# Kernel optimization log

Hardware: AMD Instinct MI355X
Metric: run time of the kernel (lower is better)

## Reference

```python
import jax, jax.numpy as jnp
import numpy as np

N, E, B = 16000, 256000, 32
IN, HID, H1, OUT, H2 = 768, 256, 4, 128, 2
LN_EPS = 1e-5


def _gat_layer(x, src, dst, W, a_src, a_dst, b, heads, out, n, concat):
    # x: (n, in), W: (heads*out, in), a_src/a_dst: (heads, out), b: (heads*out,) or (out,)
    h = (x @ W.T).reshape(n, heads, out)                      # (n, H, out)
    alpha_s = (h * a_src).sum(-1)                             # (n, H)
    alpha_d = (h * a_dst).sum(-1)                             # (n, H)
    e = jax.nn.leaky_relu(alpha_s[src] + alpha_d[dst], 0.2)   # (E', H)
    # segment softmax over incoming edges of each dst node
    m = jax.ops.segment_max(e, dst, num_segments=n)           # (n, H)
    ex = jnp.exp(e - m[dst])
    den = jax.ops.segment_sum(ex, dst, num_segments=n)
    alpha = ex / (den[dst] + 1e-16)                           # (E', H)
    msg = h[src] * alpha[..., None]                           # (E', H, out)
    agg = jax.ops.segment_sum(msg, dst, num_segments=n)       # (n, H, out)
    o = agg.reshape(n, heads * out) if concat else agg.mean(axis=1)
    return o + b


def setup_inputs() -> dict:
    key = jax.random.key(0)
    ks = jax.random.split(key, 16)
    x = jax.random.normal(ks[0], (N, IN), dtype=jnp.float32)
    edge_index = jax.random.randint(ks[1], (2, E), 0, N, dtype=jnp.int32)
    batch = jnp.sort(jax.random.randint(ks[2], (N,), 0, B, dtype=jnp.int32))
    s = 0.05
    return {
        "x": x, "edge_index": edge_index, "batch": batch,
        "W1": jax.random.normal(ks[3], (H1 * HID, IN), jnp.float32) * s,
        "a1_src": jax.random.normal(ks[4], (H1, HID), jnp.float32) * s,
        "a1_dst": jax.random.normal(ks[5], (H1, HID), jnp.float32) * s,
        "b1": jnp.zeros((H1 * HID,), jnp.float32),
        "W2": jax.random.normal(ks[6], (H2 * OUT, H1 * HID), jnp.float32) * s,
        "a2_src": jax.random.normal(ks[7], (H2, OUT), jnp.float32) * s,
        "a2_dst": jax.random.normal(ks[8], (H2, OUT), jnp.float32) * s,
        "b2": jnp.zeros((OUT,), jnp.float32),
        "proj_W": jax.random.normal(ks[9], (768, OUT), jnp.float32) * s,
        "proj_b": jnp.zeros((768,), jnp.float32),
        "ln_g": jnp.ones((768,), jnp.float32),
        "ln_b": jnp.zeros((768,), jnp.float32),
    }


def reference(x, edge_index, batch, W1, a1_src, a1_dst, b1,
              W2, a2_src, a2_dst, b2, proj_W, proj_b, ln_g, ln_b):
    # add self-loops (PyG GATConv default add_self_loops=True)
    loop = jnp.arange(N, dtype=edge_index.dtype)
    src = jnp.concatenate([edge_index[0], loop])
    dst = jnp.concatenate([edge_index[1], loop])

    h1 = jax.nn.elu(_gat_layer(x, src, dst, W1, a1_src, a1_dst, b1, H1, HID, N, True))
    # dropout = 0 (eval mode)
    h2 = jax.nn.elu(_gat_layer(h1, src, dst, W2, a2_src, a2_dst, b2, H2, OUT, N, False))

    # global mean pool per graph
    sums = jax.ops.segment_sum(h2, batch, num_segments=B)            # (B, OUT)
    cnt = jax.ops.segment_sum(jnp.ones((N,), h2.dtype), batch, num_segments=B)
    pooled = sums / jnp.maximum(cnt, 1.0)[:, None]

    z = pooled @ proj_W.T + proj_b                                   # (B, 768)
    mu = z.mean(-1, keepdims=True)
    var = ((z - mu) ** 2).mean(-1, keepdims=True)
    graph_embed = (z - mu) / jnp.sqrt(var + LN_EPS) * ln_g + ln_b
    return graph_embed, h2
```

## Files before the change

### kernel.cpp

```cpp
#include <hip/hip_runtime.h>
#include <cstddef>

#define NN   16000
#define NE   256000
#define EP   (NE + NN)
#define BG   32
#define IN_F 768
#define HID  256
#define H1C  4
#define F1   (H1C * HID)
#define OUTF 128
#define H2C  2
#define F2   (H2C * OUTF)

typedef __bf16 bf16x8 __attribute__((ext_vector_type(8)));
typedef float  f32x4  __attribute__((ext_vector_type(4)));
typedef float  f32x2  __attribute__((ext_vector_type(2)));
typedef unsigned short us8 __attribute__((ext_vector_type(8)));

static __device__ __forceinline__ float lrelu02(float x) { return x > 0.f ? x : 0.2f * x; }
static __device__ __forceinline__ float eluf(float x)    { return x > 0.f ? x : expm1f(x); }
static __device__ __forceinline__ unsigned short rne_bf16(float f) {
    unsigned u = __float_as_uint(f);
    return (unsigned short)((u + 0x7fffu + ((u >> 16) & 1u)) >> 16);
}
static __device__ __forceinline__ float b2f(unsigned short u) {
    return __uint_as_float(((unsigned)u) << 16);
}
static __device__ __forceinline__ f32x2 cvt2(unsigned int u) {
    f32x2 r;
    r.x = __uint_as_float(u << 16);
    r.y = __uint_as_float(u & 0xffff0000u);
    return r;
}

#define GLDS16(gp, lp) __builtin_amdgcn_global_load_lds(                         \
    (const __attribute__((address_space(1))) void*)(gp),                          \
    (__attribute__((address_space(3))) void*)(lp), 16, 0, 0)

#define NB_X  ((NN * IN_F) / 1024)
#define NB_W1 ((F1 * IN_F) / 1024)
#define NB_W2 ((F2 * F1) / 1024)
#define NB_H  ((EP + 255) / 256)
#define NB_PREP (NB_X + NB_W1 + NB_W2 + NB_H)

static __device__ __forceinline__ void f2b_body(const float* __restrict__ in,
                                                unsigned short* __restrict__ out,
                                                int blk, int t) {
    int i = (blk * 256 + t) * 4;
    float4 v = *(const float4*)&in[i];
    ushort4 o;
    o.x = rne_bf16(v.x); o.y = rne_bf16(v.y); o.z = rne_bf16(v.z); o.w = rne_bf16(v.w);
    *(ushort4*)&out[i] = o;
}

__global__ __launch_bounds__(256) void k_prep(const float* __restrict__ x,
                                              const float* __restrict__ W1,
                                              const float* __restrict__ W2,
                                              unsigned short* __restrict__ xb,
                                              unsigned short* __restrict__ W1b,
                                              unsigned short* __restrict__ W2b,
                                              const int* __restrict__ ei,
                                              int* __restrict__ deg) {
    int b = blockIdx.x, t = threadIdx.x;
    if (b < NB_X) { f2b_body(x, xb, b, t); return; }
    b -= NB_X;
    if (b < NB_W1) { f2b_body(W1, W1b, b, t); return; }
    b -= NB_W1;
    if (b < NB_W2) { f2b_body(W2, W2b, b, t); return; }
    b -= NB_W2;
    int e = b * 256 + t;
    if (e >= EP) return;
    int d = (e < NE) ? ei[NE + e] : (e - NE);
    atomicAdd(&deg[d], 1);
}

__global__ __launch_bounds__(1024) void k_scan(const int* __restrict__ deg,
                                               int* __restrict__ off, int* __restrict__ cursor) {
    __shared__ int sums[1024];
    int t = threadIdx.x;
    const int CH = 16;
    int base = t * CH;
    int s = 0;
    for (int i = 0; i < CH; ++i) { int idx = base + i; if (idx < NN) s += deg[idx]; }
    sums[t] = s;
    __syncthreads();
    for (int ofs = 1; ofs < 1024; ofs <<= 1) {
        int v = 0;
        if (t >= ofs) v = sums[t - ofs];
        __syncthreads();
        sums[t] += v;
        __syncthreads();
    }
    int run = sums[t] - s;
    for (int i = 0; i < CH; ++i) {
        int idx = base + i;
        if (idx < NN) { off[idx] = run; cursor[idx] = run; run += deg[idx]; }
    }
    if (t == 1023) off[NN] = run;
}

__global__ void k_scatter(const int* __restrict__ ei, int* __restrict__ cursor,
                          int* __restrict__ csr_src, int* __restrict__ csr_dst) {
    int e = blockIdx.x * 256 + threadIdx.x;
    if (e >= EP) return;
    int s, d;
    if (e < NE) { s = ei[e]; d = ei[NE + e]; } else { s = d = e - NE; }
    int pos = atomicAdd(&cursor[d], 1);
    csr_src[pos] = s;
    csr_dst[pos] = d;
}

__global__ __launch_bounds__(256) void k_mfma_nt(const unsigned short* __restrict__ A,
                                                 const unsigned short* __restrict__ B,
                                                 unsigned short* __restrict__ C,
                                                 int N, int K) {
    __shared__ __align__(16) unsigned short As[128 * 32];
    __shared__ __align__(16) unsigned short Bs[128 * 32];
    const int t = threadIdx.x;
    const int w = t >> 6, lane = t & 63;
    const int m0 = blockIdx.y * 128, n0 = blockIdx.x * 128;
    const int wm = (w >> 1) * 64, wn = (w & 1) * 64;

    const unsigned short* ga0 = A + (size_t)(m0 + (t >> 2)) * K + (t & 3) * 8;
    const unsigned short* ga1 = ga0 + (size_t)64 * K;
    const unsigned short* gb0 = B + (size_t)(n0 + (t >> 2)) * K + (t & 3) * 8;
    const unsigned short* gb1 = gb0 + (size_t)64 * K;
    unsigned short* lA0 = &As[(w * 64) * 8];
    unsigned short* lA1 = &As[(w * 64 + 256) * 8];
    unsigned short* lB0 = &Bs[(w * 64) * 8];
    unsigned short* lB1 = &Bs[(w * 64 + 256) * 8];

    f32x4 acc[4][4] = {};

    const bf16x8* pa = (const bf16x8*)As + (wm + (lane & 15)) * 4 + (lane >> 4);
    const bf16x8* pb = (const bf16x8*)Bs + (wn + (lane & 15)) * 4 + (lane >> 4);

    for (int k0 = 0; k0 < K; k0 += 32) {
        GLDS16(ga0, lA0); GLDS16(ga1, lA1);
        GLDS16(gb0, lB0); GLDS16(gb1, lB1);
        ga0 += 32; ga1 += 32; gb0 += 32; gb1 += 32;
        __syncthreads();
        bf16x8 a0 = pa[0], a1 = pa[64], a2 = pa[128], a3 = pa[192];
        bf16x8 b0 = pb[0], b1 = pb[64], b2 = pb[128], b3 = pb[192];
        acc[0][0] = __builtin_amdgcn_mfma_f32_16x16x32_bf16(a0, b0, acc[0][0], 0, 0, 0);
        acc[0][1] = __builtin_amdgcn_mfma_f32_16x16x32_bf16(a0, b1, acc[0][1], 0, 0, 0);
        acc[0][2] = __builtin_amdgcn_mfma_f32_16x16x32_bf16(a0, b2, acc[0][2], 0, 0, 0);
        acc[0][3] = __builtin_amdgcn_mfma_f32_16x16x32_bf16(a0, b3, acc[0][3], 0, 0, 0);
        acc[1][0] = __builtin_amdgcn_mfma_f32_16x16x32_bf16(a1, b0, acc[1][0], 0, 0, 0);
        acc[1][1] = __builtin_amdgcn_mfma_f32_16x16x32_bf16(a1, b1, acc[1][1], 0, 0, 0);
        acc[1][2] = __builtin_amdgcn_mfma_f32_16x16x32_bf16(a1, b2, acc[1][2], 0, 0, 0);
        acc[1][3] = __builtin_amdgcn_mfma_f32_16x16x32_bf16(a1, b3, acc[1][3], 0, 0, 0);
        acc[2][0] = __builtin_amdgcn_mfma_f32_16x16x32_bf16(a2, b0, acc[2][0], 0, 0, 0);
        acc[2][1] = __builtin_amdgcn_mfma_f32_16x16x32_bf16(a2, b1, acc[2][1], 0, 0, 0);
        acc[2][2] = __builtin_amdgcn_mfma_f32_16x16x32_bf16(a2, b2, acc[2][2], 0, 0, 0);
        acc[2][3] = __builtin_amdgcn_mfma_f32_16x16x32_bf16(a2, b3, acc[2][3], 0, 0, 0);
        acc[3][0] = __builtin_amdgcn_mfma_f32_16x16x32_bf16(a3, b0, acc[3][0], 0, 0, 0);
        acc[3][1] = __builtin_amdgcn_mfma_f32_16x16x32_bf16(a3, b1, acc[3][1], 0, 0, 0);
        acc[3][2] = __builtin_amdgcn_mfma_f32_16x16x32_bf16(a3, b2, acc[3][2], 0, 0, 0);
        acc[3][3] = __builtin_amdgcn_mfma_f32_16x16x32_bf16(a3, b3, acc[3][3], 0, 0, 0);
        __syncthreads();
    }
    const int ccol = n0 + wn + (lane & 15);
    const int crow = m0 + wm + (lane >> 4) * 4;
#pragma unroll
    for (int mi = 0; mi < 4; ++mi)
#pragma unroll
        for (int i = 0; i < 4; ++i) {
            unsigned short* cp = C + (size_t)(crow + mi * 16 + i) * N + ccol;
            cp[0]  = rne_bf16(acc[mi][0][i]);
            cp[16] = rne_bf16(acc[mi][1][i]);
            cp[32] = rne_bf16(acc[mi][2][i]);
            cp[48] = rne_bf16(acc[mi][3][i]);
        }
}

__global__ __launch_bounds__(256) void k_alpha1(const unsigned short* __restrict__ h,
                                                const float* __restrict__ a_s,
                                                const float* __restrict__ a_d,
                                                float* __restrict__ as_o,
                                                float* __restrict__ ad_o) {
    int n = blockIdx.x;
    int t = threadIdx.x;
    int head = t >> 6;
    int f = t * 4;
    ushort4 hu = *(const ushort4*)&h[(size_t)n * F1 + f];
    float4 sv = *(const float4*)&a_s[f];
    float4 dv = *(const float4*)&a_d[f];
    float hx = b2f(hu.x), hy = b2f(hu.y), hz = b2f(hu.z), hw = b2f(hu.w);
    float ps = hx * sv.x + hy * sv.y + hz * sv.z + hw * sv.w;
    float pd = hx * dv.x + hy * dv.y + hz * dv.z + hw * dv.w;
    for (int ofs = 32; ofs > 0; ofs >>= 1) {
        ps += __shfl_down(ps, ofs);
        pd += __shfl_down(pd, ofs);
    }
    if ((t & 63) == 0) { as_o[n * H1C + head] = ps; ad_o[n * H1C + head] = pd; }
}

__global__ __launch_bounds__(256) void k_alpha2(const unsigned short* __restrict__ h,
                                                const float* __restrict__ a_s,
                                                const float* __restrict__ a_d,
                                                float* __restrict__ as_o,
                                                float* __restrict__ ad_o) {
    int n = blockIdx.x * 4 + (threadIdx.x >> 6);
    int lane = threadIdx.x & 63;
    int f = lane * 4;
    ushort4 hu = *(const ushort4*)&h[(size_t)n * F2 + f];
    float4 sv = *(const float4*)&a_s[f];
    float4 dv = *(const float4*)&a_d[f];
    float hx = b2f(hu.x), hy = b2f(hu.y), hz = b2f(hu.z), hw = b2f(hu.w);
    float ps = hx * sv.x + hy * sv.y + hz * sv.z + hw * sv.w;
    float pd = hx * dv.x + hy * dv.y + hz * dv.z + hw * dv.w;
    for (int ofs = 16; ofs > 0; ofs >>= 1) {
        ps += __shfl_down(ps, ofs, 32);
        pd += __shfl_down(pd, ofs, 32);
    }
    if ((lane & 31) == 0) {
        int head = lane >> 5;
        as_o[n * H2C + head] = ps;
        ad_o[n * H2C + head] = pd;
    }
}

__global__ __launch_bounds__(256) void k_el1(const int* __restrict__ csr_src,
                                             const int* __restrict__ csr_dst,
                                             const float* __restrict__ as1,
                                             const float* __restrict__ ad1,
                                             float* __restrict__ el) {
    int j = blockIdx.x * 256 + threadIdx.x;
    if (j >= EP) return;
    int s = csr_src[j], d = csr_dst[j];
    float4 av = *(const float4*)&as1[s * H1C];
    float4 dv = *(const float4*)&ad1[d * H1C];
    float4 o;
    o.x = expf(lrelu02(av.x + dv.x));
    o.y = expf(lrelu02(av.y + dv.y));
    o.z = expf(lrelu02(av.z + dv.z));
    o.w = expf(lrelu02(av.w + dv.w));
    *(float4*)&el[(size_t)j * 4] = o;
}

__global__ __launch_bounds__(256) void k_el2(const int* __restrict__ csr_src,
                                             const int* __restrict__ csr_dst,
                                             const float* __restrict__ as2,
                                             const float* __restrict__ ad2,
                                             float* __restrict__ el) {
    int j = blockIdx.x * 256 + threadIdx.x;
    if (j >= EP) return;
    int s = csr_src[j], d = csr_dst[j];
    float2 av = *(const float2*)&as2[s * 2];
    float2 dv = *(const float2*)&ad2[d * 2];
    float2 o;
    o.x = expf(lrelu02(av.x + dv.x));
    o.y = expf(lrelu02(av.y + dv.y));
    *(float2*)&el[(size_t)j * 2] = o;
}

__global__ __launch_bounds__(256) void k_gat1(const unsigned short* __restrict__ hb,
                                              const float* __restrict__ el,
                                              const int* __restrict__ off,
                                              const int* __restrict__ csr,
                                              const float* __restrict__ b1,
                                              unsigned short* __restrict__ h1b) {
    const int l = threadIdx.x & 63;
    const int w = threadIdx.x >> 6;
    const int d = blockIdx.x * 2 + (w >> 1);
    const int hf = w & 1;
    const int beg = off[d], end = off[d + 1];
    const int h = hf * 2 + (l >> 5);
    const int f0 = hf * 512 + l * 8;

    float sA = 0.f, sB = 0.f;
    for (int j = beg + l; j < end; j += 64) {
        float2 e = *(const float2*)&el[(size_t)j * 4 + hf * 2];
        sA += e.x; sB += e.y;
    }
    for (int o = 32; o > 0; o >>= 1) {
        sA += __shfl_down(sA, o);
        sB += __shfl_down(sB, o);
    }
    sA = __shfl(sA, 0); sB = __shfl(sB, 0);
    float rdh = 1.f / (((l < 32) ? sA : sB) + 1e-16f);

    f32x2 acc[4] = {};
    const unsigned int* hbase = (const unsigned int*)hb;
    const int lofs = f0 >> 1;
    for (int cbeg = beg; cbeg < end; cbeg += 32) {
        int cnt = end - cbeg; if (cnt > 32) cnt = 32;
        int idx = cbeg + (l & 31);
        int idxc = idx < end ? idx : end - 1;
        int s_sel = csr[idxc];
        float ev = el[(size_t)idxc * 4 + h];
        float myw = (idx < end) ? ev * rdh : 0.f;
        for (int jj = 0; jj < cnt; jj += 4) {
            int sa = __builtin_amdgcn_readlane(s_sel, jj + 0);
            int sb = __builtin_amdgcn_readlane(s_sel, jj + 1);
            int sc = __builtin_amdgcn_readlane(s_sel, jj + 2);
            int sd = __builtin_amdgcn_readlane(s_sel, jj + 3);
            float wa = __shfl(myw, (l & 32) | (jj + 0));
            float wb = __shfl(myw, (l & 32) | (jj + 1));
            float wc = __shfl(myw, (l & 32) | (jj + 2));
            float wd = __shfl(myw, (l & 32) | (jj + 3));
            uint4 va = *(const uint4*)(hbase + (unsigned)sa * (F1 / 2) + lofs);
            uint4 vb = *(const uint4*)(hbase + (unsigned)sb * (F1 / 2) + lofs);
            uint4 vc = *(const uint4*)(hbase + (unsigned)sc * (F1 / 2) + lofs);
            uint4 vd = *(const uint4*)(hbase + (unsigned)sd * (F1 / 2) + lofs);
            f32x2 wa2 = {wa, wa}, wb2 = {wb, wb}, wc2 = {wc, wc}, wd2 = {wd, wd};
            acc[0] += wa2 * cvt2(va.x); acc[1] += wa2 * cvt2(va.y);
            acc[2] += wa2 * cvt2(va.z); acc[3] += wa2 * cvt2(va.w);
            acc[0] += wb2 * cvt2(vb.x); acc[1] += wb2 * cvt2(vb.y);
            acc[2] += wb2 * cvt2(vb.z); acc[3] += wb2 * cvt2(vb.w);
            acc[0] += wc2 * cvt2(vc.x); acc[1] += wc2 * cvt2(vc.y);
            acc[2] += wc2 * cvt2(vc.z); acc[3] += wc2 * cvt2(vc.w);
            acc[0] += wd2 * cvt2(vd.x); acc[1] += wd2 * cvt2(vd.y);
            acc[2] += wd2 * cvt2(vd.z); acc[3] += wd2 * cvt2(vd.w);
        }
    }
    us8 ob;
#pragma unroll
    for (int i = 0; i < 4; ++i) {
        ob[2 * i]     = rne_bf16(eluf(acc[i].x + b1[f0 + 2 * i]));
        ob[2 * i + 1] = rne_bf16(eluf(acc[i].y + b1[f0 + 2 * i + 1]));
    }
    *(us8*)&h1b[(size_t)d * F1 + f0] = ob;
}

__global__ __launch_bounds__(256) void k_gat2(const unsigned short* __restrict__ h2b,
                                              const float* __restrict__ el,
                                              const int* __restrict__ off,
                                              const int* __restrict__ csr,
                                              const float* __restrict__ b2,
                                              float* __restrict__ out_h2) {
    const int l = threadIdx.x & 63;
    const int d = blockIdx.x * 4 + (threadIdx.x >> 6);
    const int beg = off[d], end = off[d + 1];
    const int c = l & 31, p = l >> 5;
    const int myhead = c >> 4;
    const int hw = p;

    float s0 = 0.f, s1 = 0.f;
    for (int j = beg + l; j < end; j += 64) {
        float2 e = *(const float2*)&el[(size_t)j * 2];
        s0 += e.x; s1 += e.y;
    }
    for (int o = 32; o > 0; o >>= 1) {
        s0 += __shfl_down(s0, o);
        s1 += __shfl_down(s1, o);
    }
    s0 = __shfl(s0, 0); s1 = __shfl(s1, 0);
    float rdhw = 1.f / ((hw ? s1 : s0) + 1e-16f);

    f32x2 acc[4] = {};
    const unsigned int* base = (const unsigned int*)h2b + c * 4;
    for (int cbeg = beg; cbeg < end; cbeg += 32) {
        int cnt = end - cbeg; if (cnt > 32) cnt = 32;
        int idx = cbeg + c;
        int idxc = idx < end ? idx : end - 1;
        int s_sel = csr[idxc];
        float ev = el[(size_t)idxc * 2 + hw];
        float myw = (idx < end) ? ev * rdhw : 0.f;
        for (int jj = 0; jj < cnt; jj += 8) {
            int e0 = jj + p * 4;
            int sa = __shfl(s_sel, e0 + 0);
            int sb = __shfl(s_sel, e0 + 1);
            int sc = __shfl(s_sel, e0 + 2);
            int sd = __shfl(s_sel, e0 + 3);
            float wa = __shfl(myw, (myhead << 5) | (e0 + 0));
            float wb = __shfl(myw, (myhead << 5) | (e0 + 1));
            float wc = __shfl(myw, (myhead << 5) | (e0 + 2));
            float wd = __shfl(myw, (myhead << 5) | (e0 + 3));
            uint4 va = *(const uint4*)(base + (unsigned)sa * (F2 / 2));
            uint4 vb = *(const uint4*)(base + (unsigned)sb * (F2 / 2));
            uint4 vc = *(const uint4*)(base + (unsigned)sc * (F2 / 2));
            uint4 vd = *(const uint4*)(base + (unsigned)sd * (F2 / 2));
            f32x2 wa2 = {wa, wa}, wb2 = {wb, wb}, wc2 = {wc, wc}, wd2 = {wd, wd};
            acc[0] += wa2 * cvt2(va.x); acc[1] += wa2 * cvt2(va.y);
            acc[2] += wa2 * cvt2(va.z); acc[3] += wa2 * cvt2(va.w);
            acc[0] += wb2 * cvt2(vb.x); acc[1] += wb2 * cvt2(vb.y);
            acc[2] += wb2 * cvt2(vb.z); acc[3] += wb2 * cvt2(vb.w);
            acc[0] += wc2 * cvt2(vc.x); acc[1] += wc2 * cvt2(vc.y);
            acc[2] += wc2 * cvt2(vc.z); acc[3] += wc2 * cvt2(vc.w);
            acc[0] += wd2 * cvt2(vd.x); acc[1] += wd2 * cvt2(vd.y);
            acc[2] += wd2 * cvt2(vd.z); acc[3] += wd2 * cvt2(vd.w);
        }
    }
    float af[8] = {acc[0].x, acc[0].y, acc[1].x, acc[1].y,
                   acc[2].x, acc[2].y, acc[3].x, acc[3].y};
#pragma unroll
    for (int i = 0; i < 8; ++i) af[i] += __shfl(af[i], l ^ 32);
    float pt[8];
#pragma unroll
    for (int i = 0; i < 8; ++i) pt[i] = __shfl(af[i], l ^ 16);
    if (l < 16) {
        int f = l * 8;
        float o[8];
#pragma unroll
        for (int i = 0; i < 8; ++i) o[i] = eluf(0.5f * (af[i] + pt[i]) + b2[f + i]);
        *(float4*)&out_h2[(size_t)d * OUTF + f]     = make_float4(o[0], o[1], o[2], o[3]);
        *(float4*)&out_h2[(size_t)d * OUTF + f + 4] = make_float4(o[4], o[5], o[6], o[7]);
    }
}

__global__ __launch_bounds__(1024) void k_proj_ln(const float* __restrict__ h2,
                                                  const int* __restrict__ batch,
                                                  const float* __restrict__ pW,
                                                  const float* __restrict__ pb,
                                                  const float* __restrict__ g,
                                                  const float* __restrict__ be,
                                                  float* __restrict__ out) {
    __shared__ float part[1024];
    __shared__ float ph[OUTF];
    __shared__ float zb[768];
    __shared__ float red[1024];
    __shared__ float s_mu, s_rstd;
    int b = blockIdx.x, t = threadIdx.x;
    int lo = 0, hi = NN;
    while (lo < hi) { int mid = (lo + hi) >> 1; if (batch[mid] < b) lo = mid + 1; else hi = mid; }
    int n0 = lo;
    lo = 0; hi = NN;
    while (lo < hi) { int mid = (lo + hi) >> 1; if (batch[mid] < b + 1) lo = mid + 1; else hi = mid; }
    int n1 = lo;
    {
        int f = t & 127, slot = t >> 7;
        float a = 0.f;
        for (int n = n0 + slot; n < n1; n += 8) a += h2[(size_t)n * OUTF + f];
        part[t] = a;
    }
    __syncthreads();
    if (t < OUTF) {
        float s = 0.f;
#pragma unroll
        for (int k = 0; k < 8; ++k) s += part[k * 128 + t];
        float c = (float)(n1 - n0);
        c = c < 1.f ? 1.f : c;
        ph[t] = s / c;
    }
    __syncthreads();
    if (t < 768) {
        float acc = pb[t];
        for (int k = 0; k < OUTF; k += 4) {
            float4 w = *(const float4*)&pW[(size_t)t * OUTF + k];
            acc += w.x * ph[k] + w.y * ph[k + 1] + w.z * ph[k + 2] + w.w * ph[k + 3];
        }
        zb[t] = acc;
    }
    __syncthreads();
    red[t] = (t < 768) ? zb[t] : 0.f;
    __syncthreads();
    for (int ofs = 512; ofs > 0; ofs >>= 1) {
        if (t < ofs) red[t] += red[t + ofs];
        __syncthreads();
    }
    if (t == 0) s_mu = red[0] / 768.f;
    __syncthreads();
    float mu = s_mu;
    float dv = (t < 768) ? (zb[t] - mu) : 0.f;
    red[t] = dv * dv;
    __syncthreads();
    for (int ofs = 512; ofs > 0; ofs >>= 1) {
        if (t < ofs) red[t] += red[t + ofs];
        __syncthreads();
    }
    if (t == 0) s_rstd = rsqrtf(red[0] / 768.f + 1e-5f);
    __syncthreads();
    float rstd = s_rstd;
    if (t < 768)
        out[(size_t)b * 768 + t] = (zb[t] - mu) * rstd * g[t] + be[t];
}

extern "C" void kernel_launch(void* const* d_in, const int* in_sizes, int n_in,
                              void* d_out, int out_size, void* d_ws, size_t ws_size,
                              hipStream_t stream) {
    const float* x    = (const float*)d_in[0];
    const int*   ei   = (const int*)d_in[1];
    const int*   batch= (const int*)d_in[2];
    const float* W1   = (const float*)d_in[3];
    const float* a1s  = (const float*)d_in[4];
    const float* a1d  = (const float*)d_in[5];
    const float* b1   = (const float*)d_in[6];
    const float* W2   = (const float*)d_in[7];
    const float* a2s  = (const float*)d_in[8];
    const float* a2d  = (const float*)d_in[9];
    const float* b2   = (const float*)d_in[10];
    const float* pW   = (const float*)d_in[11];
    const float* pb   = (const float*)d_in[12];
    const float* lng  = (const float*)d_in[13];
    const float* lnb  = (const float*)d_in[14];

    float* out_ge = (float*)d_out;
    float* out_h2 = (float*)d_out + BG * 768;

    char* w = (char*)d_ws;
    unsigned short* xb   = (unsigned short*)w;  w += (size_t)NN * IN_F * 2;
    unsigned short* W1b  = (unsigned short*)w;  w += (size_t)F1 * IN_F * 2;
    unsigned short* W2b  = (unsigned short*)w;  w += (size_t)F2 * F1 * 2;
    unsigned short* hbufb= (unsigned short*)w;  w += (size_t)NN * F1 * 2;
    unsigned short* h1b  = (unsigned short*)w;  w += (size_t)NN * F1 * 2;
    unsigned short* h2b  = (unsigned short*)w;  w += (size_t)NN * F2 * 2;
    float* as1  = (float*)w;  w += (size_t)NN * H1C * 4;
    float* ad1  = (float*)w;  w += (size_t)NN * H1C * 4;
    float* as2  = (float*)w;  w += (size_t)NN * H2C * 4;
    float* ad2  = (float*)w;  w += (size_t)NN * H2C * 4;
    int* deg    = (int*)w;    w += (size_t)NN * 4;
    int* off    = (int*)w;    w += (size_t)(NN + 4) * 4;
    int* cursor = (int*)w;    w += (size_t)NN * 4;
    int* csr    = (int*)w;    w += (size_t)EP * 4;
    int* csrd   = (int*)w;    w += (size_t)EP * 4;
    float* el1  = (float*)w;  w += (size_t)EP * H1C * 4;
    float* el2  = (float*)w;  w += (size_t)EP * H2C * 4;

    hipMemsetAsync(deg, 0, NN * 4, stream);

    k_prep<<<NB_PREP, 256, 0, stream>>>(x, W1, W2, xb, W1b, W2b, ei, deg);
    k_scan<<<1, 1024, 0, stream>>>(deg, off, cursor);
    k_scatter<<<(EP + 255) / 256, 256, 0, stream>>>(ei, cursor, csr, csrd);

    k_mfma_nt<<<dim3(F1 / 128, NN / 128), 256, 0, stream>>>(xb, W1b, hbufb, F1, IN_F);
    k_alpha1<<<NN, 256, 0, stream>>>(hbufb, a1s, a1d, as1, ad1);
    k_el1<<<(EP + 255) / 256, 256, 0, stream>>>(csr, csrd, as1, ad1, el1);
    k_gat1<<<NN / 2, 256, 0, stream>>>(hbufb, el1, off, csr, b1, h1b);

    k_mfma_nt<<<dim3(F2 / 128, NN / 128), 256, 0, stream>>>(h1b, W2b, h2b, F2, F1);
    k_alpha2<<<NN / 4, 256, 0, stream>>>(h2b, a2s, a2d, as2, ad2);
    k_el2<<<(EP + 255) / 256, 256, 0, stream>>>(csr, csrd, as2, ad2, el2);
    k_gat2<<<NN / 4, 256, 0, stream>>>(h2b, el2, off, csr, b2, out_h2);

    k_proj_ln<<<BG, 1024, 0, stream>>>(out_h2, batch, pW, pb, lng, lnb, out_ge);
}
```

Measured before the change: 414.5 us.

## Fuse attention-score dot products into GEMM epilogue and merge edge scatter into GEMM1

The per-node attention dot products (alpha_src/alpha_dst) are now computed in the GEMM epilogue from fp32 accumulators, using wave shuffles and atomicAdd into zeroed buffers. This removes the separate alpha kernels and their reread of h. The CSR edge scatter runs as extra blocks of the first GEMM launch, so the two overlap and one launch is saved. The GEMM K loop now loads 64 columns per iteration instead of 32, halving the barrier count, and a single memset zeroes the alpha accumulators together with deg. In exchange, atomics add contention and make the float summation order nondeterministic, and the alpha values now come from unrounded fp32 rather than the bf16-stored h.

```diff
diff --git a/kernel.cpp b/kernel.cpp
--- a/kernel.cpp
+++ b/kernel.cpp
@@ -23,9 +23,6 @@
 static __device__ __forceinline__ unsigned short rne_bf16(float f) {
     unsigned u = __float_as_uint(f);
     return (unsigned short)((u + 0x7fffu + ((u >> 16) & 1u)) >> 16);
-}
-static __device__ __forceinline__ float b2f(unsigned short u) {
-    return __uint_as_float(((unsigned)u) << 16);
 }
 static __device__ __forceinline__ f32x2 cvt2(unsigned int u) {
     f32x2 r;
@@ -100,65 +97,73 @@
     if (t == 1023) off[NN] = run;
 }
 
-__global__ void k_scatter(const int* __restrict__ ei, int* __restrict__ cursor,
-                          int* __restrict__ csr_src, int* __restrict__ csr_dst) {
-    int e = blockIdx.x * 256 + threadIdx.x;
-    if (e >= EP) return;
-    int s, d;
-    if (e < NE) { s = ei[e]; d = ei[NE + e]; } else { s = d = e - NE; }
-    int pos = atomicAdd(&cursor[d], 1);
-    csr_src[pos] = s;
-    csr_dst[pos] = d;
-}
-
-__global__ __launch_bounds__(256) void k_mfma_nt(const unsigned short* __restrict__ A,
+template <int KITER, int HSHIFT, int HCNT>
+static __device__ __forceinline__ void gemm_body(const unsigned short* __restrict__ A,
                                                  const unsigned short* __restrict__ B,
                                                  unsigned short* __restrict__ C,
-                                                 int N, int K) {
-    __shared__ __align__(16) unsigned short As[128 * 32];
-    __shared__ __align__(16) unsigned short Bs[128 * 32];
-    const int t = threadIdx.x;
+                                                 const float* __restrict__ a_s,
+                                                 const float* __restrict__ a_d,
+                                                 float* __restrict__ as_o,
+                                                 float* __restrict__ ad_o,
+                                                 int N, int K, int bx, int by,
+                                                 unsigned short* As, unsigned short* Bs,
+                                                 int t) {
     const int w = t >> 6, lane = t & 63;
-    const int m0 = blockIdx.y * 128, n0 = blockIdx.x * 128;
+    const int m0 = by * 128, n0 = bx * 128;
     const int wm = (w >> 1) * 64, wn = (w & 1) * 64;
 
-    const unsigned short* ga0 = A + (size_t)(m0 + (t >> 2)) * K + (t & 3) * 8;
-    const unsigned short* ga1 = ga0 + (size_t)64 * K;
-    const unsigned short* gb0 = B + (size_t)(n0 + (t >> 2)) * K + (t & 3) * 8;
-    const unsigned short* gb1 = gb0 + (size_t)64 * K;
-    unsigned short* lA0 = &As[(w * 64) * 8];
-    unsigned short* lA1 = &As[(w * 64 + 256) * 8];
-    unsigned short* lB0 = &Bs[(w * 64) * 8];
-    unsigned short* lB1 = &Bs[(w * 64 + 256) * 8];
+    const unsigned short* ga = A + (size_t)(m0 + (t >> 2)) * K + (t & 3) * 8;
+    const unsigned short* gb = B + (size_t)(n0 + (t >> 2)) * K + (t & 3) * 8;
+    unsigned short* lA0 = As + (w * 64) * 8;
+    unsigned short* lA0b = As + (w * 64 + 256) * 8;
+    unsigned short* lA1 = As + 4096 + (w * 64) * 8;
+    unsigned short* lA1b = As + 4096 + (w * 64 + 256) * 8;
+    unsigned short* lB0 = Bs + (w * 64) * 8;
+    unsigned short* lB0b = Bs + (w * 64 + 256) * 8;
+    unsigned short* lB1 = Bs + 4096 + (w * 64) * 8;
+    unsigned short* lB1b = Bs + 4096 + (w * 64 + 256) * 8;
 
     f32x4 acc[4][4] = {};
 
-    const bf16x8* pa = (const bf16x8*)As + (wm + (lane & 15)) * 4 + (lane >> 4);
-    const bf16x8* pb = (const bf16x8*)Bs + (wn + (lane & 15)) * 4 + (lane >> 4);
-
-    for (int k0 = 0; k0 < K; k0 += 32) {
-        GLDS16(ga0, lA0); GLDS16(ga1, lA1);
-        GLDS16(gb0, lB0); GLDS16(gb1, lB1);
-        ga0 += 32; ga1 += 32; gb0 += 32; gb1 += 32;
+    const bf16x8* pa0 = (const bf16x8*)As + (wm + (lane & 15)) * 4 + (lane >> 4);
+    const bf16x8* pa1 = (const bf16x8*)(As + 4096) + (wm + (lane & 15)) * 4 + (lane >> 4);
+    const bf16x8* pb0 = (const bf16x8*)Bs + (wn + (lane & 15)) * 4 + (lane >> 4);
+    const bf16x8* pb1 = (const bf16x8*)(Bs + 4096) + (wn + (lane & 15)) * 4 + (lane >> 4);
+
+    for (int it = 0; it < KITER; ++it) {
+        GLDS16(ga, lA0);
+        GLDS16(ga + (size_t)64 * K, lA0b);
+        GLDS16(ga + 32, lA1);
+        GLDS16(ga + 32 + (size_t)64 * K, lA1b);
+        GLDS16(gb, lB0);
+        GLDS16(gb + (size_t)64 * K, lB0b);
+        GLDS16(gb + 32, lB1);
+        GLDS16(gb + 32 + (size_t)64 * K, lB1b);
+        ga += 64; gb += 64;
         __syncthreads();
-        bf16x8 a0 = pa[0], a1 = pa[64], a2 = pa[128], a3 = pa[192];
-        bf16x8 b0 = pb[0], b1 = pb[64], b2 = pb[128], b3 = pb[192];
-        acc[0][0] = __builtin_amdgcn_mfma_f32_16x16x32_bf16(a0, b0, acc[0][0], 0, 0, 0);
-        acc[0][1] = __builtin_amdgcn_mfma_f32_16x16x32_bf16(a0, b1, acc[0][1], 0, 0, 0);
-        acc[0][2] = __builtin_amdgcn_mfma_f32_16x16x32_bf16(a0, b2, acc[0][2], 0, 0, 0);
-        acc[0][3] = __builtin_amdgcn_mfma_f32_16x16x32_bf16(a0, b3, acc[0][3], 0, 0, 0);
-        acc[1][0] = __builtin_amdgcn_mfma_f32_16x16x32_bf16(a1, b0, acc[1][0], 0, 0, 0);
-        acc[1][1] = __builtin_amdgcn_mfma_f32_16x16x32_bf16(a1, b1, acc[1][1], 0, 0, 0);
-        acc[1][2] = __builtin_amdgcn_mfma_f32_16x16x32_bf16(a1, b2, acc[1][2], 0, 0, 0);
-        acc[1][3] = __builtin_amdgcn_mfma_f32_16x16x32_bf16(a1, b3, acc[1][3], 0, 0, 0);
-        acc[2][0] = __builtin_amdgcn_mfma_f32_16x16x32_bf16(a2, b0, acc[2][0], 0, 0, 0);
-        acc[2][1] = __builtin_amdgcn_mfma_f32_16x16x32_bf16(a2, b1, acc[2][1], 0, 0, 0);
-        acc[2][2] = __builtin_amdgcn_mfma_f32_16x16x32_bf16(a2, b2, acc[2][2], 0, 0, 0);
-        acc[2][3] = __builtin_amdgcn_mfma_f32_16x16x32_bf16(a2, b3, acc[2][3], 0, 0, 0);
-        acc[3][0] = __builtin_amdgcn_mfma_f32_16x16x32_bf16(a3, b0, acc[3][0], 0, 0, 0);
-        acc[3][1] = __builtin_amdgcn_mfma_f32_16x16x32_bf16(a3, b1, acc[3][1], 0, 0, 0);
-        acc[3][2] = __builtin_amdgcn_mfma_f32_16x16x32_bf16(a3, b2, acc[3][2], 0, 0, 0);
-        acc[3][3] = __builtin_amdgcn_mfma_f32_16x16x32_bf16(a3, b3, acc[3][3], 0, 0, 0);
+#pragma unroll
+        for (int kk = 0; kk < 2; ++kk) {
+            const bf16x8* pa = kk ? pa1 : pa0;
+            const bf16x8* pb = kk ? pb1 : pb0;
+            bf16x8 a0 = pa[0], a1 = pa[64], a2 = pa[128], a3 = pa[192];
+            bf16x8 b0 = pb[0], b1 = pb[64], b2 = pb[128], b3 = pb[192];
+            acc[0][0] = __builtin_amdgcn_mfma_f32_16x16x32_bf16(a0, b0, acc[0][0], 0, 0, 0);
+            acc[0][1] = __builtin_amdgcn_mfma_f32_16x16x32_bf16(a0, b1, acc[0][1], 0, 0, 0);
+            acc[0][2] = __builtin_amdgcn_mfma_f32_16x16x32_bf16(a0, b2, acc[0][2], 0, 0, 0);
+            acc[0][3] = __builtin_amdgcn_mfma_f32_16x16x32_bf16(a0, b3, acc[0][3], 0, 0, 0);
+            acc[1][0] = __builtin_amdgcn_mfma_f32_16x16x32_bf16(a1, b0, acc[1][0], 0, 0, 0);
+            acc[1][1] = __builtin_amdgcn_mfma_f32_16x16x32_bf16(a1, b1, acc[1][1], 0, 0, 0);
+            acc[1][2] = __builtin_amdgcn_mfma_f32_16x16x32_bf16(a1, b2, acc[1][2], 0, 0, 0);
+            acc[1][3] = __builtin_amdgcn_mfma_f32_16x16x32_bf16(a1, b3, acc[1][3], 0, 0, 0);
+            acc[2][0] = __builtin_amdgcn_mfma_f32_16x16x32_bf16(a2, b0, acc[2][0], 0, 0, 0);
+            acc[2][1] = __builtin_amdgcn_mfma_f32_16x16x32_bf16(a2, b1, acc[2][1], 0, 0, 0);
+            acc[2][2] = __builtin_amdgcn_mfma_f32_16x16x32_bf16(a2, b2, acc[2][2], 0, 0, 0);
+            acc[2][3] = __builtin_amdgcn_mfma_f32_16x16x32_bf16(a2, b3, acc[2][3], 0, 0, 0);
+            acc[3][0] = __builtin_amdgcn_mfma_f32_16x16x32_bf16(a3, b0, acc[3][0], 0, 0, 0);
+            acc[3][1] = __builtin_amdgcn_mfma_f32_16x16x32_bf16(a3, b1, acc[3][1], 0, 0, 0);
+            acc[3][2] = __builtin_amdgcn_mfma_f32_16x16x32_bf16(a3, b2, acc[3][2], 0, 0, 0);
+            acc[3][3] = __builtin_amdgcn_mfma_f32_16x16x32_bf16(a3, b3, acc[3][3], 0, 0, 0);
+        }
         __syncthreads();
     }
     const int ccol = n0 + wn + (lane & 15);
@@ -173,53 +178,73 @@
             cp[32] = rne_bf16(acc[mi][2][i]);
             cp[48] = rne_bf16(acc[mi][3][i]);
         }
-}
-
-__global__ __launch_bounds__(256) void k_alpha1(const unsigned short* __restrict__ h,
-                                                const float* __restrict__ a_s,
-                                                const float* __restrict__ a_d,
-                                                float* __restrict__ as_o,
-                                                float* __restrict__ ad_o) {
-    int n = blockIdx.x;
-    int t = threadIdx.x;
-    int head = t >> 6;
-    int f = t * 4;
-    ushort4 hu = *(const ushort4*)&h[(size_t)n * F1 + f];
-    float4 sv = *(const float4*)&a_s[f];
-    float4 dv = *(const float4*)&a_d[f];
-    float hx = b2f(hu.x), hy = b2f(hu.y), hz = b2f(hu.z), hw = b2f(hu.w);
-    float ps = hx * sv.x + hy * sv.y + hz * sv.z + hw * sv.w;
-    float pd = hx * dv.x + hy * dv.y + hz * dv.z + hw * dv.w;
-    for (int ofs = 32; ofs > 0; ofs >>= 1) {
-        ps += __shfl_down(ps, ofs);
-        pd += __shfl_down(pd, ofs);
-    }
-    if ((t & 63) == 0) { as_o[n * H1C + head] = ps; ad_o[n * H1C + head] = pd; }
-}
-
-__global__ __launch_bounds__(256) void k_alpha2(const unsigned short* __restrict__ h,
-                                                const float* __restrict__ a_s,
-                                                const float* __restrict__ a_d,
-                                                float* __restrict__ as_o,
-                                                float* __restrict__ ad_o) {
-    int n = blockIdx.x * 4 + (threadIdx.x >> 6);
-    int lane = threadIdx.x & 63;
-    int f = lane * 4;
-    ushort4 hu = *(const ushort4*)&h[(size_t)n * F2 + f];
-    float4 sv = *(const float4*)&a_s[f];
-    float4 dv = *(const float4*)&a_d[f];
-    float hx = b2f(hu.x), hy = b2f(hu.y), hz = b2f(hu.z), hw = b2f(hu.w);
-    float ps = hx * sv.x + hy * sv.y + hz * sv.z + hw * sv.w;
-    float pd = hx * dv.x + hy * dv.y + hz * dv.z + hw * dv.w;
-    for (int ofs = 16; ofs > 0; ofs >>= 1) {
-        ps += __shfl_down(ps, ofs, 32);
-        pd += __shfl_down(pd, ofs, 32);
-    }
-    if ((lane & 31) == 0) {
-        int head = lane >> 5;
-        as_o[n * H2C + head] = ps;
-        ad_o[n * H2C + head] = pd;
-    }
+    const int hh = n0 >> HSHIFT;
+    float asv[4], adv[4];
+#pragma unroll
+    for (int bi = 0; bi < 4; ++bi) {
+        asv[bi] = a_s[ccol + bi * 16];
+        adv[bi] = a_d[ccol + bi * 16];
+    }
+#pragma unroll
+    for (int mi = 0; mi < 4; ++mi)
+#pragma unroll
+        for (int i = 0; i < 4; ++i) {
+            float vs = acc[mi][0][i] * asv[0] + acc[mi][1][i] * asv[1]
+                     + acc[mi][2][i] * asv[2] + acc[mi][3][i] * asv[3];
+            float vd = acc[mi][0][i] * adv[0] + acc[mi][1][i] * adv[1]
+                     + acc[mi][2][i] * adv[2] + acc[mi][3][i] * adv[3];
+#pragma unroll
+            for (int m = 1; m <= 8; m <<= 1) {
+                vs += __shfl_xor(vs, m);
+                vd += __shfl_xor(vd, m);
+            }
+            if ((lane & 15) == 0) {
+                int r = crow + mi * 16 + i;
+                atomicAdd(&as_o[r * HCNT + hh], vs);
+                atomicAdd(&ad_o[r * HCNT + hh], vd);
+            }
+        }
+}
+
+#define G1_BLKS (8 * 125)
+__global__ __launch_bounds__(256) void k_gemm1(const unsigned short* __restrict__ A,
+                                               const unsigned short* __restrict__ B,
+                                               unsigned short* __restrict__ C,
+                                               const float* __restrict__ a_s,
+                                               const float* __restrict__ a_d,
+                                               float* __restrict__ as_o,
+                                               float* __restrict__ ad_o,
+                                               const int* __restrict__ ei,
+                                               int* __restrict__ cursor,
+                                               int* __restrict__ csr_src,
+                                               int* __restrict__ csr_dst) {
+    __shared__ __align__(16) unsigned short As[8192];
+    __shared__ __align__(16) unsigned short Bs[8192];
+    int blk = blockIdx.x, t = threadIdx.x;
+    if (blk < G1_BLKS) {
+        gemm_body<12, 8, 4>(A, B, C, a_s, a_d, as_o, ad_o, F1, IN_F, blk & 7, blk >> 3, As, Bs, t);
+        return;
+    }
+    int e = (blk - G1_BLKS) * 256 + t;
+    if (e >= EP) return;
+    int s, d;
+    if (e < NE) { s = ei[e]; d = ei[NE + e]; } else { s = d = e - NE; }
+    int pos = atomicAdd(&cursor[d], 1);
+    csr_src[pos] = s;
+    csr_dst[pos] = d;
+}
+
+__global__ __launch_bounds__(256) void k_gemm2(const unsigned short* __restrict__ A,
+                                               const unsigned short* __restrict__ B,
+                                               unsigned short* __restrict__ C,
+                                               const float* __restrict__ a_s,
+                                               const float* __restrict__ a_d,
+                                               float* __restrict__ as_o,
+                                               float* __restrict__ ad_o) {
+    __shared__ __align__(16) unsigned short As[8192];
+    __shared__ __align__(16) unsigned short Bs[8192];
+    gemm_body<16, 7, 2>(A, B, C, a_s, a_d, as_o, ad_o, F2, F1,
+                        blockIdx.x, blockIdx.y, As, Bs, threadIdx.x);
 }
 
 __global__ __launch_bounds__(256) void k_el1(const int* __restrict__ csr_src,
@@ -509,19 +534,17 @@
     float* el1  = (float*)w;  w += (size_t)EP * H1C * 4;
     float* el2  = (float*)w;  w += (size_t)EP * H2C * 4;
 
-    hipMemsetAsync(deg, 0, NN * 4, stream);
+    hipMemsetAsync(as1, 0, (size_t)NN * (H1C + H1C + H2C + H2C + 1) * 4, stream);
 
     k_prep<<<NB_PREP, 256, 0, stream>>>(x, W1, W2, xb, W1b, W2b, ei, deg);
     k_scan<<<1, 1024, 0, stream>>>(deg, off, cursor);
-    k_scatter<<<(EP + 255) / 256, 256, 0, stream>>>(ei, cursor, csr, csrd);
-
-    k_mfma_nt<<<dim3(F1 / 128, NN / 128), 256, 0, stream>>>(xb, W1b, hbufb, F1, IN_F);
-    k_alpha1<<<NN, 256, 0, stream>>>(hbufb, a1s, a1d, as1, ad1);
+
+    k_gemm1<<<G1_BLKS + NB_H, 256, 0, stream>>>(xb, W1b, hbufb, a1s, a1d, as1, ad1,
+                                                ei, cursor, csr, csrd);
     k_el1<<<(EP + 255) / 256, 256, 0, stream>>>(csr, csrd, as1, ad1, el1);
     k_gat1<<<NN / 2, 256, 0, stream>>>(hbufb, el1, off, csr, b1, h1b);
 
-    k_mfma_nt<<<dim3(F2 / 128, NN / 128), 256, 0, stream>>>(h1b, W2b, h2b, F2, F1);
-    k_alpha2<<<NN / 4, 256, 0, stream>>>(h2b, a2s, a2d, as2, ad2);
+    k_gemm2<<<dim3(F2 / 128, NN / 128), 256, 0, stream>>>(h1b, W2b, h2b, a2s, a2d, as2, ad2);
     k_el2<<<(EP + 255) / 256, 256, 0, stream>>>(csr, csrd, as2, ad2, el2);
     k_gat2<<<NN / 4, 256, 0, stream>>>(h2b, el2, off, csr, b2, out_h2);
 
```

After: 414.1 us. About the same (-0.1%).
